# Performance work log

Hardware: AMD Instinct MI355X
Metric: run time of the kernel (lower is better)

The kernel has to match this reference:

```python
import jax, jax.numpy as jnp
import numpy as np

B, T, C = 2, 2048, 1024
H = 16
D = C // H
SCALE = 0.1 / (D ** 0.5)  # nonstandard 0.1/sqrt(head_dim) scale from source


def setup_inputs() -> dict:
    key = jax.random.key(0)
    ks = jax.random.split(key, 5)
    s = 0.02
    return {
        "x": jax.random.normal(ks[0], (B, T, C), jnp.float32),
        "w_attn": jax.random.normal(ks[1], (C, 3 * C), jnp.float32) * s,
        "b_attn": jax.random.normal(ks[2], (3 * C,), jnp.float32) * s,
        "w_proj": jax.random.normal(ks[3], (C, C), jnp.float32) * s,
        "b_proj": jax.random.normal(ks[4], (C,), jnp.float32) * s,
    }


def reference(x, w_attn, b_attn, w_proj, b_proj):
    Bs, Ts, Cs = x.shape
    qkv = x @ w_attn + b_attn                      # [B,T,3C]
    q, k, v = jnp.split(qkv, 3, axis=-1)
    q = q.reshape(Bs, Ts, H, D)                    # [B,T,H,D]
    k = k.reshape(Bs, Ts, H, D)
    v = v.reshape(Bs, Ts, H, D)
    attn = jnp.einsum("bthd,bshd->bhts", q, k) * SCALE  # [B,H,T,T]
    causal = jnp.tril(jnp.ones((Ts, Ts), dtype=bool))
    attn = jnp.where(causal, attn, -jnp.inf)
    attn = jax.nn.softmax(attn, axis=-1)
    y = jnp.einsum("bhts,bshd->bthd", attn, v).reshape(Bs, Ts, Cs)
    return y @ w_proj + b_proj
```

## Files before the change

### kernel.cpp

```cpp
#include <hip/hip_runtime.h>


#define Bz 2
#define Tz 2048
#define Cz 1024
#define Hz 16
#define Dz 64
#define QSCALE 0.01803368801111437f

typedef unsigned short u16;
typedef short bf16x8 __attribute__((ext_vector_type(8)));
typedef float f32x4 __attribute__((ext_vector_type(4)));

#define MFMA32(A, B, C) __builtin_amdgcn_mfma_f32_16x16x32_bf16(A, B, C, 0, 0, 0)

__device__ inline u16 f2bf(float f) {
  return (u16)((__float_as_uint(f) + 0x8000u) >> 16);
}

__device__ inline float fexp2(float x) {
  return exp2f(x);
}

__device__ inline void gl_lds16(const u16* g, u16* l) {
  __builtin_amdgcn_global_load_lds(
      (const __attribute__((address_space(1))) void*)g,
      (__attribute__((address_space(3))) void*)l, 16, 0, 0);
}

#define NCAST 4096
#define NTA   3072
__global__ __launch_bounds__(256) void prep_kernel(const float* __restrict__ x,
                                                   const float* __restrict__ wa,
                                                   const float* __restrict__ wp,
                                                   u16* __restrict__ xb,
                                                   u16* __restrict__ waT,
                                                   u16* __restrict__ wpT) {
  const int bx = blockIdx.x, t = threadIdx.x;
  if (bx < NCAST) {
    int i = bx * 256 + t;
    float4 v = ((const float4*)x)[i];
    ushort4 o = {f2bf(v.x), f2bf(v.y), f2bf(v.z), f2bf(v.w)};
    ((ushort4*)xb)[i] = o;
    return;
  }
  __shared__ float tile[32][33];
  const float* W;
  u16* WT;
  int N, idx;
  if (bx < NCAST + NTA) {
    W = wa; WT = waT; N = 3 * Cz; idx = bx - NCAST;
  } else {
    W = wp; WT = wpT; N = Cz; idx = bx - NCAST - NTA;
  }
  const int n0 = (idx % (N / 32)) * 32, k0 = (idx / (N / 32)) * 32;
  const int tx = t & 31, ty = t >> 5;
#pragma unroll
  for (int i = 0; i < 4; ++i)
    tile[ty + 8 * i][tx] = W[(size_t)(k0 + ty + 8 * i) * N + n0 + tx];
  __syncthreads();
#pragma unroll
  for (int i = 0; i < 4; ++i)
    WT[(size_t)(n0 + ty + 8 * i) * Cz + k0 + tx] = f2bf(tile[tx][ty + 8 * i]);
}

template <bool OUT_BF16, int TN>
__global__ __launch_bounds__(256) void gemm_bt(const u16* __restrict__ A,
                                               const u16* __restrict__ BT,
                                               const float* __restrict__ bias,
                                               void* __restrict__ Cout,
                                               int M, int N, int K,
                                               int qcols, float qscale) {
  __shared__ __align__(16) u16 As[128 * 64];
  __shared__ __align__(16) u16 Bs[TN * 64];
  constexpr int NT = TN / 32;
  const int t = threadIdx.x;
  const int wave = t >> 6, lane = t & 63;
  const int lm = lane & 15, lg = lane >> 4;
  const int wm = wave >> 1, wn = wave & 1;
  const int m0 = blockIdx.y * 128, n0 = blockIdx.x * TN;

  const int lrow = lane >> 3;
  const int gseg = (lane & 7) ^ lrow;
  const size_t a_base = (size_t)(m0 + 32 * wave + lrow) * K + gseg * 8;
  u16* const a_lds = &As[(32 * wave) * 64];
  const size_t b_base = (size_t)(n0 + (TN / 4) * wave + lrow) * K + gseg * 8;
  u16* const b_lds = &Bs[((TN / 4) * wave) * 64];

  f32x4 acc[4][NT];
#pragma unroll
  for (int mt = 0; mt < 4; ++mt)
#pragma unroll
    for (int nt = 0; nt < NT; ++nt)
#pragma unroll
      for (int i = 0; i < 4; ++i) acc[mt][nt][i] = 0.f;

  for (int k0 = 0; k0 < K; k0 += 64) {
    __syncthreads();
#pragma unroll
    for (int i = 0; i < 4; ++i)
      gl_lds16(A + a_base + (size_t)(8 * i) * K + k0, a_lds + i * 8 * 64);
#pragma unroll
    for (int i = 0; i < NT; ++i)
      gl_lds16(BT + b_base + (size_t)(8 * i) * K + k0, b_lds + i * 8 * 64);
    __syncthreads();

#pragma unroll
    for (int h = 0; h < 2; ++h) {
      const int rs = ((lg + 4 * h) ^ (lm & 7)) * 8;
      bf16x8 af[4], bfr[NT];
#pragma unroll
      for (int mt = 0; mt < 4; ++mt)
        af[mt] = *(const bf16x8*)&As[(64 * wm + 16 * mt + lm) * 64 + rs];
#pragma unroll
      for (int nt = 0; nt < NT; ++nt)
        bfr[nt] = *(const bf16x8*)&Bs[((TN / 2) * wn + 16 * nt + lm) * 64 + rs];
#pragma unroll
      for (int mt = 0; mt < 4; ++mt)
#pragma unroll
        for (int nt = 0; nt < NT; ++nt)
          acc[mt][nt] = MFMA32(af[mt], bfr[nt], acc[mt][nt]);
    }
  }

#pragma unroll
  for (int nt = 0; nt < NT; ++nt) {
    int gc = n0 + (TN / 2) * wn + 16 * nt + lm;
    float bv = bias[gc];
    float sc = (gc < qcols) ? qscale : 1.f;
#pragma unroll
    for (int mt = 0; mt < 4; ++mt) {
#pragma unroll
      for (int i = 0; i < 4; ++i) {
        int gr = m0 + 64 * wm + 16 * mt + 4 * lg + i;
        float v = (acc[mt][nt][i] + bv) * sc;
        if (OUT_BF16)
          ((u16*)Cout)[(size_t)gr * N + gc] = f2bf(v);
        else
          ((float*)Cout)[(size_t)gr * N + gc] = v;
      }
    }
  }
}

__global__ __launch_bounds__(256) void attn_kernel(const u16* __restrict__ qkv,
                                                   u16* __restrict__ yb) {
  __shared__ __align__(16) u16 Ks[64][72];
  __shared__ __align__(16) u16 Vt[64][72];
  __shared__ __align__(16) u16 Ps[64][72];

  const int t = threadIdx.x;
  const int wave = t >> 6, lane = t & 63;
  const int lm = lane & 15, lg = lane >> 4;
  const int kg8 = lg << 3;
  const int x = blockIdx.x;
  const int bh = x & 31, qtp = x >> 5;
  const int qt = (qtp < 16) ? qtp : 47 - qtp;
  const int b = bh >> 4, h = bh & 15;
  const int q0 = qt * 64;
  const size_t rowstride = 3 * Cz;
  const u16* qbase = qkv + (size_t)b * Tz * rowstride + h * Dz;

  bf16x8 qf[2];
  {
    const u16* qrow = qbase + (size_t)(q0 + wave * 16 + lm) * rowstride + kg8;
    qf[0] = *(const bf16x8*)qrow;
    qf[1] = *(const bf16x8*)(qrow + 32);
  }

  float psum[4];
  f32x4 Oa[4];
#pragma unroll
  for (int i = 0; i < 4; ++i) {
    psum[i] = 0.f;
#pragma unroll
    for (int j = 0; j < 4; ++j) Oa[i][j] = 0.f;
  }

  const int ksr = t >> 2, kds = (t & 3) << 4;
  const int vsp = t & 31, vds = (t >> 5) << 3;
  const u16* kbase = qbase + Cz + (size_t)ksr * rowstride + kds;
  const u16* vbase = qbase + 2 * Cz + (size_t)(2 * vsp) * rowstride + vds;
  const size_t tilestep = 64 * rowstride;

  uint4 krA[2], vrA[2], krB[2], vrB[2];
  {
    krA[0] = *(const uint4*)kbase;
    krA[1] = *(const uint4*)(kbase + 8);
    vrA[0] = *(const uint4*)vbase;
    vrA[1] = *(const uint4*)(vbase + rowstride);
    const size_t t1 = (qt >= 1) ? tilestep : 0;
    krB[0] = *(const uint4*)(kbase + t1);
    krB[1] = *(const uint4*)(kbase + t1 + 8);
    vrB[0] = *(const uint4*)(vbase + t1);
    vrB[1] = *(const uint4*)(vbase + t1 + rowstride);
  }

  auto stage = [&](uint4 (&kr)[2], uint4 (&vr)[2], int ktc) {
    __syncthreads();
    *(uint4*)&Ks[ksr][kds] = kr[0];
    *(uint4*)&Ks[ksr][kds + 8] = kr[1];
    {
      unsigned av[4] = {vr[0].x, vr[0].y, vr[0].z, vr[0].w};
      unsigned cv[4] = {vr[1].x, vr[1].y, vr[1].z, vr[1].w};
#pragma unroll
      for (int j = 0; j < 4; ++j) {
        unsigned w0 = (av[j] & 0xffffu) | (cv[j] << 16);
        unsigned w1 = (av[j] >> 16) | (cv[j] & 0xffff0000u);
        *(unsigned*)&Vt[vds + 2 * j][2 * vsp] = w0;
        *(unsigned*)&Vt[vds + 2 * j + 1][2 * vsp] = w1;
      }
    }
    __syncthreads();

    if (ktc + 2 <= qt) {
      const u16* kp = kbase + (size_t)(ktc + 2) * tilestep;
      const u16* vp = vbase + (size_t)(ktc + 2) * tilestep;
      kr[0] = *(const uint4*)kp;
      kr[1] = *(const uint4*)(kp + 8);
      vr[0] = *(const uint4*)vp;
      vr[1] = *(const uint4*)(vp + rowstride);
    }

    f32x4 S[4];
#pragma unroll
    for (int c = 0; c < 4; ++c) {
      bf16x8 k0 = *(const bf16x8*)&Ks[c * 16 + lm][kg8];
      bf16x8 k1 = *(const bf16x8*)&Ks[c * 16 + lm][32 + kg8];
      f32x4 s;
#pragma unroll
      for (int i = 0; i < 4; ++i) s[i] = 0.f;
      s = MFMA32(qf[0], k0, s);
      s = MFMA32(qf[1], k1, s);
      S[c] = s;
    }

    const bool diag = (ktc == qt);
#pragma unroll
    for (int c = 0; c < 4; ++c) {
#pragma unroll
      for (int r = 0; r < 4; ++r) {
        float p = fexp2(S[c][r]);
        if (diag && (c * 16 + lm) > (16 * wave + 4 * lg + r)) p = 0.f;
        psum[r] += p;
        Ps[16 * wave + 4 * lg + r][c * 16 + lm] = f2bf(p);
      }
    }

    bf16x8 pf0 = *(const bf16x8*)&Ps[16 * wave + lm][kg8];
    bf16x8 pf1 = *(const bf16x8*)&Ps[16 * wave + lm][32 + kg8];
#pragma unroll
    for (int c = 0; c < 4; ++c) {
      bf16x8 v0 = *(const bf16x8*)&Vt[c * 16 + lm][kg8];
      bf16x8 v1 = *(const bf16x8*)&Vt[c * 16 + lm][32 + kg8];
      Oa[c] = MFMA32(pf0, v0, Oa[c]);
      Oa[c] = MFMA32(pf1, v1, Oa[c]);
    }
  };

  for (int kt = 0; kt <= qt; kt += 2) {
    stage(krA, vrA, kt);
    if (kt + 1 <= qt) stage(krB, vrB, kt + 1);
  }

  float inv[4];
#pragma unroll
  for (int r = 0; r < 4; ++r) {
    float s = psum[r];
#pragma unroll
    for (int msk = 1; msk < 16; msk <<= 1) s += __shfl_xor(s, msk);
    inv[r] = 1.f / s;
  }
#pragma unroll
  for (int c = 0; c < 4; ++c)
#pragma unroll
    for (int r = 0; r < 4; ++r)
      Ps[16 * wave + 4 * lg + r][c * 16 + lm] = f2bf(Oa[c][r] * inv[r]);

  {
    const int row = lane >> 2, seg = lane & 3;
    const uint4* src = (const uint4*)&Ps[16 * wave + row][seg * 16];
    uint4 v0 = src[0];
    uint4 v1 = src[1];
    u16* dst = yb + (size_t)(b * Tz + q0 + 16 * wave + row) * Cz + h * Dz + seg * 16;
    *(uint4*)dst = v0;
    *(uint4*)(dst + 8) = v1;
  }
}

extern "C" void kernel_launch(void* const* d_in, const int* in_sizes, int n_in,
                              void* d_out, int out_size, void* d_ws, size_t ws_size,
                              hipStream_t stream) {
  const float* x      = (const float*)d_in[0];
  const float* w_attn = (const float*)d_in[1];
  const float* b_attn = (const float*)d_in[2];
  const float* w_proj = (const float*)d_in[3];
  const float* b_proj = (const float*)d_in[4];

  char* ws = (char*)d_ws;
  u16* xb   = (u16*)(ws);
  u16* waT  = (u16*)(ws + (8ull << 20));
  u16* wpT  = (u16*)(ws + (14ull << 20));
  u16* qkvb = (u16*)(ws + (16ull << 20));
  u16* yb   = (u16*)(ws + (40ull << 20));

  const int M = Bz * Tz;

  prep_kernel<<<NCAST + NTA + 1024, 256, 0, stream>>>(x, w_attn, w_proj, xb, waT, wpT);
  gemm_bt<true, 128><<<dim3(3 * Cz / 128, M / 128), 256, 0, stream>>>(
      xb, waT, b_attn, qkvb, M, 3 * Cz, Cz, Cz, QSCALE);
  attn_kernel<<<1024, 256, 0, stream>>>(qkvb, yb);
  gemm_bt<false, 64><<<dim3(Cz / 64, M / 128), 256, 0, stream>>>(
      yb, wpT, b_proj, d_out, M, Cz, Cz, 0, 1.f);
}
```

Measured before the change: 212.0 us.

## Keep attention probabilities in registers by transposing the QK MFMA operands

Swaps the operands of the QK^T MFMA so the score fragment lands in the layout the PV MFMA wants as its A operand. This removes the LDS round-trip of the P tile, and PV now uses 16x16x16 bf16 MFMAs fed directly from registers. The row-sum reduction changes to match the new layout, the final normalisation reuses the Ks buffer with added barriers, and exp2 goes through the hardware builtin. The cost is twice as many, smaller MFMAs for PV and Vt reads with a different access pattern.

```diff
diff --git a/kernel.cpp b/kernel.cpp
--- a/kernel.cpp
+++ b/kernel.cpp
@@ -9,17 +9,30 @@
 #define QSCALE 0.01803368801111437f
 
 typedef unsigned short u16;
+typedef short bf16x4 __attribute__((ext_vector_type(4)));
 typedef short bf16x8 __attribute__((ext_vector_type(8)));
 typedef float f32x4 __attribute__((ext_vector_type(4)));
 
 #define MFMA32(A, B, C) __builtin_amdgcn_mfma_f32_16x16x32_bf16(A, B, C, 0, 0, 0)
 
+__device__ inline f32x4 mfma16(bf16x4 a, bf16x4 b, f32x4 c) {
+#if defined(__HIP_DEVICE_COMPILE__)
+  return __builtin_amdgcn_mfma_f32_16x16x16bf16_1k(a, b, c, 0, 0, 0);
+#else
+  return c;
+#endif
+}
+
 __device__ inline u16 f2bf(float f) {
   return (u16)((__float_as_uint(f) + 0x8000u) >> 16);
 }
 
 __device__ inline float fexp2(float x) {
+#if __has_builtin(__builtin_amdgcn_exp2f)
+  return __builtin_amdgcn_exp2f(x);
+#else
   return exp2f(x);
+#endif
 }
 
 __device__ inline void gl_lds16(const u16* g, u16* l) {
@@ -147,7 +160,6 @@
                                                    u16* __restrict__ yb) {
   __shared__ __align__(16) u16 Ks[64][72];
   __shared__ __align__(16) u16 Vt[64][72];
-  __shared__ __align__(16) u16 Ps[64][72];
 
   const int t = threadIdx.x;
   const int wave = t >> 6, lane = t & 63;
@@ -168,14 +180,12 @@
     qf[1] = *(const bf16x8*)(qrow + 32);
   }
 
-  float psum[4];
+  float psum = 0.f;
   f32x4 Oa[4];
 #pragma unroll
-  for (int i = 0; i < 4; ++i) {
-    psum[i] = 0.f;
+  for (int i = 0; i < 4; ++i)
 #pragma unroll
     for (int j = 0; j < 4; ++j) Oa[i][j] = 0.f;
-  }
 
   const int ksr = t >> 2, kds = (t & 3) << 4;
   const int vsp = t & 31, vds = (t >> 5) << 3;
@@ -230,31 +240,32 @@
       f32x4 s;
 #pragma unroll
       for (int i = 0; i < 4; ++i) s[i] = 0.f;
-      s = MFMA32(qf[0], k0, s);
-      s = MFMA32(qf[1], k1, s);
+      s = MFMA32(k0, qf[0], s);
+      s = MFMA32(k1, qf[1], s);
       S[c] = s;
     }
 
     const bool diag = (ktc == qt);
+    const int qloc = 16 * wave + lm;
+    bf16x4 pf[4];
 #pragma unroll
     for (int c = 0; c < 4; ++c) {
 #pragma unroll
       for (int r = 0; r < 4; ++r) {
         float p = fexp2(S[c][r]);
-        if (diag && (c * 16 + lm) > (16 * wave + 4 * lg + r)) p = 0.f;
-        psum[r] += p;
-        Ps[16 * wave + 4 * lg + r][c * 16 + lm] = f2bf(p);
+        if (diag && (c * 16 + 4 * lg + r) > qloc) p = 0.f;
+        psum += p;
+        pf[c][r] = (short)f2bf(p);
       }
     }
 
-    bf16x8 pf0 = *(const bf16x8*)&Ps[16 * wave + lm][kg8];
-    bf16x8 pf1 = *(const bf16x8*)&Ps[16 * wave + lm][32 + kg8];
-#pragma unroll
-    for (int c = 0; c < 4; ++c) {
-      bf16x8 v0 = *(const bf16x8*)&Vt[c * 16 + lm][kg8];
-      bf16x8 v1 = *(const bf16x8*)&Vt[c * 16 + lm][32 + kg8];
-      Oa[c] = MFMA32(pf0, v0, Oa[c]);
-      Oa[c] = MFMA32(pf1, v1, Oa[c]);
+#pragma unroll
+    for (int dt = 0; dt < 4; ++dt) {
+#pragma unroll
+      for (int c = 0; c < 4; ++c) {
+        bf16x4 vfr = *(const bf16x4*)&Vt[16 * dt + lm][c * 16 + 4 * lg];
+        Oa[dt] = mfma16(pf[c], vfr, Oa[dt]);
+      }
     }
   };
 
@@ -263,23 +274,24 @@
     if (kt + 1 <= qt) stage(krB, vrB, kt + 1);
   }
 
-  float inv[4];
-#pragma unroll
-  for (int r = 0; r < 4; ++r) {
-    float s = psum[r];
-#pragma unroll
-    for (int msk = 1; msk < 16; msk <<= 1) s += __shfl_xor(s, msk);
-    inv[r] = 1.f / s;
-  }
-#pragma unroll
-  for (int c = 0; c < 4; ++c)
+  float s = psum;
+  s += __shfl_xor(s, 16);
+  s += __shfl_xor(s, 32);
+  const float linv = 1.f / s;
+  float invq[4];
+#pragma unroll
+  for (int r = 0; r < 4; ++r)
+    invq[r] = __shfl(linv, 20 * lg + r);
+  __syncthreads();
+#pragma unroll
+  for (int dt = 0; dt < 4; ++dt)
 #pragma unroll
     for (int r = 0; r < 4; ++r)
-      Ps[16 * wave + 4 * lg + r][c * 16 + lm] = f2bf(Oa[c][r] * inv[r]);
-
+      Ks[16 * wave + 4 * lg + r][16 * dt + lm] = f2bf(Oa[dt][r] * invq[r]);
+  __syncthreads();
   {
     const int row = lane >> 2, seg = lane & 3;
-    const uint4* src = (const uint4*)&Ps[16 * wave + row][seg * 16];
+    const uint4* src = (const uint4*)&Ks[16 * wave + row][seg * 16];
     uint4 v0 = src[0];
     uint4 v1 = src[1];
     u16* dst = yb + (size_t)(b * Tz + q0 + 16 * wave + row) * Cz + h * Dz + seg * 16;
```

After: 207.9 us. Within noise of the previous version (-2.0%).
